# Optimization experiments

Hardware: AMD Instinct MI355X
Metric: run time of the kernel (lower is better)

The kernel has to match this reference:

```python
import jax, jax.numpy as jnp
import numpy as np
from jax.scipy.special import logsumexp

B, T, V, C, H, D, SPW, NC = 16, 256, 10000, 4096, 256, 256, 32, 128


def _res(x, w1, b1, w2, b2):
    # ResLayer: x + relu(lin2(relu(lin1(x))))
    return x + jax.nn.relu(jax.nn.relu(x @ w1 + b1) @ w2 + b2)


def _log_phi(x, proj):
    # Performer-style log random features for the softmax kernel (smp param.)
    return x @ proj - 0.5 * jnp.sum(x * x, -1, keepdims=True)


def _log_matmul_exp(a, b):
    # logits[i,j] = logsumexp_d(a[i,d] + b[j,d]), stable, via a single GEMM
    ma = jnp.max(a, -1, keepdims=True)
    mb = jnp.max(b, -1, keepdims=True)
    return jnp.log(jnp.exp(a - ma) @ jnp.exp(b - mb).T) + ma + mb.T


def setup_inputs() -> dict:
    key = jax.random.key(0)
    ks = jax.random.split(key, 12)
    s = 1.0 / np.sqrt(H)  # xavier-ish scale
    inp = {
        "text": jax.random.randint(ks[0], (B, T), 0, V),
        "start_emb": jax.random.normal(ks[1], (H,), jnp.float32) * s,
        "start_w": jax.random.normal(ks[2], (5, H, H), jnp.float32) * s,
        "start_b": jnp.zeros((5, H), jnp.float32),
        "state_emb": jax.random.normal(ks[3], (C, H), jnp.float32) * s,
        "next_state_emb": jax.random.normal(ks[4], (C, H), jnp.float32) * s,
        "preterminal_emb": jax.random.normal(ks[5], (C, H), jnp.float32) * s,
        "terminal_w": jax.random.normal(ks[6], (4, H, H), jnp.float32) * s,
        "terminal_b": jnp.zeros((4, H), jnp.float32),
        "terminal_emb": jax.random.normal(ks[7], (V, H), jnp.float32) * s,
        "projection": jax.random.normal(ks[8], (H, D), jnp.float32),
    }
    # brown-cluster style assignment: each cluster owns SPW disjoint states
    w2c = jax.random.randint(ks[9], (V,), 0, NC)
    c2s = jnp.arange(NC)[:, None] * SPW + jnp.arange(SPW)[None, :]
    inp["word2state"] = c2s[w2c]  # [V, SPW]
    return inp


def reference(text, word2state, start_emb, start_w, start_b, state_emb,
              next_state_emb, preterminal_emb, terminal_w, terminal_b,
              terminal_emb, projection):
    # --- start distribution (tie_start=True uses next_state_emb) ---
    fx = start_emb @ start_w[0] + start_b[0]
    fx = _res(fx, start_w[1], start_b[1], start_w[2], start_b[2])
    fx = _res(fx, start_w[3], start_b[3], start_w[4], start_b[4])
    lpy = _log_phi(next_state_emb, projection)                      # [C, D]
    start_lp = jax.nn.log_softmax(
        _log_matmul_exp(_log_phi(fx[None], projection), lpy)[0])    # [C]
    # --- transition: kernelized low-rank logits, row log-softmax ---
    trans_lp = jax.nn.log_softmax(
        _log_matmul_exp(_log_phi(state_emb, projection), lpy), -1)  # [C, C]
    # --- emission: terminal_mlp + sparse word2state mask ---
    fp = _res(preterminal_emb, terminal_w[0], terminal_b[0], terminal_w[1], terminal_b[1])
    fp = _res(fp, terminal_w[2], terminal_b[2], terminal_w[3], terminal_b[3])
    emit_logits = _log_matmul_exp(_log_phi(fp, projection),
                                  _log_phi(terminal_emb, projection))  # [C, V]
    rows = word2state.reshape(-1)
    cols = jnp.repeat(jnp.arange(V), SPW)
    mask = jnp.zeros((C, V), bool).at[rows, cols].set(True)
    emit_lp = jax.nn.log_softmax(jnp.where(mask, emit_logits, -1e30), -1)
    # --- log-space forward algorithm over clamped sparse states ---
    clamped = word2state[text]                          # [B, T, SPW]
    emit_bt = emit_lp[clamped, text[:, :, None]]        # [B, T, SPW]
    alpha0 = start_lp[clamped[:, 0]] + emit_bt[:, 0]    # [B, SPW]
    xs = (jnp.swapaxes(clamped[:, :-1], 0, 1),
          jnp.swapaxes(clamped[:, 1:], 0, 1),
          jnp.swapaxes(emit_bt[:, 1:], 0, 1))

    def step(alpha, x):
        cp, cc, em = x                                   # [B,SPW] each / em [B,SPW]
        tr = trans_lp[cp[:, :, None], cc[:, None, :]]    # [B, SPW, SPW]
        return logsumexp(alpha[:, :, None] + tr, axis=1) + em, None

    alpha, _ = jax.lax.scan(step, alpha0, xs)
    return logsumexp(alpha, -1)                          # [B] log evidence
```

## Files before the change

kernel.cpp:

```cpp
#include <hip/hip_runtime.h>

#define B_   16
#define T_   256
#define V_   10000
#define C_   4096
#define H_   256
#define NC_  128
#define CAP_ 224
#define MST  33
#define XST  257
#define HST  264

typedef __bf16 bf16x8 __attribute__((ext_vector_type(8)));
typedef unsigned short u16x8 __attribute__((ext_vector_type(8)));
typedef float  f32x4  __attribute__((ext_vector_type(4)));

__device__ inline unsigned short f2bf(float f){
  unsigned int u = __float_as_uint(f);
  u += 0x7FFFu + ((u >> 16) & 1u);
  return (unsigned short)(u >> 16);
}
__device__ inline float bf2f(unsigned short u){
  return __uint_as_float(((unsigned int)u) << 16);
}
__device__ inline f32x4 mfma16(bf16x8 a, bf16x8 b, f32x4 c){
  return __builtin_amdgcn_mfma_f32_16x16x32_bf16(a, b, c, 0, 0, 0);
}
__device__ inline bf16x8 load_cvt8(const float* p){
  u16x8 u;
  #pragma unroll
  for (int i = 0; i < 8; ++i) u[i] = f2bf(p[i]);
  return __builtin_bit_cast(bf16x8, u);
}
__device__ inline void zero_acc(f32x4 acc[2][4]){
  #pragma unroll
  for (int i = 0; i < 2; ++i)
    #pragma unroll
    for (int jx = 0; jx < 4; ++jx) acc[i][jx] = (f32x4){0.f,0.f,0.f,0.f};
}

__device__ inline void fx_accum(const float* __restrict__ W, const float* xh,
                                int j, float* __restrict__ Anext){
  int t = threadIdx.x;
  float p = 0.f;
  #pragma unroll
  for (int i = 0; i < 8; ++i)
    p = fmaf(xh[i], W[(size_t)(8*j + i)*256 + t], p);
  atomicAdd(&Anext[t], p);
}

__device__ inline void mm_A_gf32(const float* __restrict__ A, size_t lda_row0,
    const unsigned short* __restrict__ Bt, int w, int ln, f32x4 acc[2][4]){
  int m16 = ln & 15, q = ln >> 4, c0 = w*64;
  const float* a0 = A + lda_row0 + (size_t)m16*256 + q*8;
  const float* a1 = a0 + 16*256;
  const unsigned short* bp0 = Bt + (size_t)(c0 + m16)*256 + q*8;
  #pragma unroll
  for (int kt = 0; kt < 8; ++kt){
    bf16x8 af0 = load_cvt8(a0 + kt*32);
    bf16x8 af1 = load_cvt8(a1 + kt*32);
    #pragma unroll
    for (int cj = 0; cj < 4; ++cj){
      bf16x8 bfj = *(const bf16x8*)(bp0 + (size_t)cj*16*256 + kt*32);
      acc[0][cj] = mfma16(af0, bfj, acc[0][cj]);
// ... 201 lines not shown
  int tid = threadIdx.x;
  int w = tid >> 6, ln = tid & 63;
  int m16 = ln & 15, q = ln >> 4;
  int c0 = w*64;
  #pragma unroll
  for (int ri = 0; ri < 2; ++ri){
    #pragma unroll
    for (int r = 0; r < 4; ++r){
      int row = ri*16 + q*4 + r;
      float mv = -1e30f;
      #pragma unroll
      for (int cj = 0; cj < 4; ++cj){
        acc[ri][cj][r] -= lnrm[row];
        mv = fmaxf(mv, acc[ri][cj][r]);
      }
      #pragma unroll
      for (int d = 1; d < 16; d <<= 1) mv = fmaxf(mv, __shfl_xor(mv, d));
      if (m16 == 0) wrow[w][row] = mv;
    }
  }
  __syncthreads();
  #pragma unroll
  for (int ri = 0; ri < 2; ++ri){
    #pragma unroll
    for (int r = 0; r < 4; ++r){
      int row = ri*16 + q*4 + r;
      int grow = r0 + row;
      float m = fmaxf(fmaxf(wrow[0][row], wrow[1][row]), fmaxf(wrow[2][row], wrow[3][row]));
      if (grow < M){
        #pragma unroll
        for (int cj = 0; cj < 4; ++cj){
          int col = c0 + cj*16 + m16;
          E[(size_t)grow*256 + col] = f2bf(__expf(acc[ri][cj][r] - m));
        }
        if (w == 0 && m16 == 0) mr[grow] = m;
      }
    }
  }
}

__device__ inline void dev_phiE(const float* __restrict__ A,
    const unsigned short* __restrict__ projT, unsigned short* __restrict__ E,
    float* __restrict__ mr, int M, int r0, float* lnrm, float (*wrow)[32])
{
  int tid = threadIdx.x;
  int w = tid >> 6, ln = tid & 63;
  f32x4 acc[2][4];
  zero_acc(acc);
  phi_core(A, projT, r0, M, w, ln, acc, lnrm);
  __syncthreads();
  phiE_epilogue(acc, E, mr, M, r0, lnrm, wrow);
}

__global__ __launch_bounds__(256) void k_prep(
  const float* __restrict__ proj, const float* __restrict__ tw,
  unsigned short* __restrict__ projT, unsigned short* __restrict__ WT,
  const int* __restrict__ w2s, int* __restrict__ cnt, int* __restrict__ list,
  const float* __restrict__ se, const float* __restrict__ sw,
  float* __restrict__ Afx)
{
  int bx = blockIdx.x, tid = threadIdx.x;
  if (bx < 1280){
    int z = bx >> 8, dcol = bx & 255;
    const float* src = (z == 0) ? proj : (tw + (size_t)(z-1)*65536);
    unsigned short* dst = (z == 0) ? projT : (WT + (size_t)(z-1)*65536);
    dst[dcol*256 + tid] = f2bf(src[tid*256 + dcol]);
    return;
  }
  if (bx < 1320){
    int v = (bx - 1280)*256 + tid;
    if (v < V_){
      int k = w2s[v*32] >> 5;
      int pos = atomicAdd(&cnt[k], 1);
      if (pos < CAP_) list[k*CAP_ + pos] = v;
    }
    return;
  }
  int j = bx - 1320;
  float xh[8];
  #pragma unroll
  for (int i = 0; i < 8; ++i) xh[i] = se[8*j + i];
  fx_accum(sw, xh, j, Afx);
}

__global__ __launch_bounds__(256) void k_stageB(
  const float* __restrict__ pre_emb, const unsigned short* __restrict__ WT,
  const float* __restrict__ term_b,
  const unsigned short* __restrict__ projT,
  unsigned short* __restrict__ Epb, float* __restrict__ mpp,
  const float* __restrict__ next_emb, unsigned short* __restrict__ Ebp,
  float* __restrict__ S,
  const float* __restrict__ term_emb, unsigned short* __restrict__ Etb,
  float* __restrict__ mt,
  const float* __restrict__ sw, const float* __restrict__ sb,
  float* __restrict__ Afx)
{
  __shared__ __align__(16) float sX[32*XST];
  __shared__ __align__(16) unsigned short sHb[32*HST];
  __shared__ float lnrm[32];
  __shared__ float wrow[4][32];
  int bx = blockIdx.x, tid = threadIdx.x;
  int w = tid >> 6, ln = tid & 63;
  int m16 = ln & 15, q = ln >> 4;
  int c0 = w*64;
  if (bx < 128){
    int r0 = bx*32;
    f32x4 acc[2][4];
    zero_acc(acc);
    mm_A_gf32(pre_emb, (size_t)r0*256, WT, w, ln, acc);
    #pragma unroll
    for (int ri = 0; ri < 2; ++ri)
      #pragma unroll
      for (int cj = 0; cj < 4; ++cj)
        #pragma unroll
        for (int r = 0; r < 4; ++r){
          int row = ri*16 + q*4 + r, col = c0 + cj*16 + m16;
          sHb[row*HST + col] = f2bf(fmaxf(acc[ri][cj][r] + term_b[col], 0.f));
        }
    __syncthreads();
    zero_acc(acc);
    mm_A_ldsbf(sHb, WT + 65536, w, ln, acc);
    #pragma unroll
    for (int ri = 0; ri < 2; ++ri)
      #pragma unroll
      for (int cj = 0; cj < 4; ++cj)
        #pragma unroll
        for (int r = 0; r < 4; ++r){
          int row = ri*16 + q*4 + r, col = c0 + cj*16 + m16;
          float v = fmaxf(acc[ri][cj][r] + term_b[256 + col], 0.f);
          sX[row*XST + col] = v + pre_emb[(size_t)(r0 + row)*256 + col];
        }
    __syncthreads();
    zero_acc(acc);
    mm_A_ldsf32(sX, WT + 2*65536, w, ln, acc, nullptr);
    __syncthreads();
    #pragma unroll
    for (int ri = 0; ri < 2; ++ri)
      #pragma unroll
      for (int cj = 0; cj < 4; ++cj)
        #pragma unroll
        for (int r = 0; r < 4; ++r){
          int row = ri*16 + q*4 + r, col = c0 + cj*16 + m16;
          sHb[row*HST + col] = f2bf(fmaxf(acc[ri][cj][r] + term_b[512 + col], 0.f));
        }
    __syncthreads();
    zero_acc(acc);
    mm_A_ldsbf(sHb, WT + 3*65536, w, ln, acc);
    #pragma unroll
    for (int ri = 0; ri < 2; ++ri)
      #pragma unroll
      for (int cj = 0; cj < 4; ++cj)
        #pragma unroll
        for (int r = 0; r < 4; ++r){
          int row = ri*16 + q*4 + r, col = c0 + cj*16 + m16;
          sX[row*XST + col] += fmaxf(acc[ri][cj][r] + term_b[768 + col], 0.f);
        }
    __syncthreads();
    zero_acc(acc);
    mm_A_ldsf32(sX, projT, w, ln, acc, lnrm);
    __syncthreads();
    phiE_epilogue(acc, Epb, mpp, C_, r0, lnrm, wrow);
  } else if (bx < 256){
    dev_phiB(next_emb, projT, Ebp, S, (bx - 128)*32, lnrm);
  } else if (bx < 569){
    dev_phiE(term_emb, projT, Etb, mt, V_, (bx - 256)*32, lnrm, wrow);
  } else {
    int j = bx - 569;
    float xh[8];
    #pragma unroll
    for (int i = 0; i < 8; ++i){ int h = 8*j + i; xh[i] = Afx[h] + sb[h]; }
    fx_accum(sw + 65536, xh, j, Afx + 256);
  }
}

__global__ __launch_bounds__(256) void k_stageC(
  const float* __restrict__ state_emb, const unsigned short* __restrict__ projT,
  const float* __restrict__ S, unsigned short* __restrict__ Eap,
  const unsigned short* __restrict__ Epb, const float* __restrict__ mpp,
  const unsigned short* __restrict__ Etb, const float* __restrict__ mt,
  const int* __restrict__ cnt, const int* __restrict__ list,
  float* __restrict__ emit_col,
  const float* __restrict__ sw, const float* __restrict__ sb,
  float* __restrict__ Afx)
{
  __shared__ float lnrm[32];
  __shared__ float sS[256];
  __shared__ float wrow[4][32];
  __shared__ float wden[4][32];
  __shared__ float mtile[8][32];
  __shared__ float stile[8][32];
  __shared__ float mpl[32];
  __shared__ float denl[32];
  int bx = blockIdx.x, tid = threadIdx.x;
  if (bx < 128){
    dev_phiA(state_emb, projT, S, Eap, bx*32, lnrm, sS, wrow, wden);
    return;
  }
  if (bx >= 256){
    int j = bx - 256;
    float xh[8];
    #pragma unroll
    for (int i = 0; i < 8; ++i){ int h = 8*j + i; xh[i] = fmaxf(Afx[256 + h] + sb[256 + h], 0.f); }
    fx_accum(sw + 2*65536, xh, j, Afx + 512);
    return;
  }
  int k = bx - 128;
  int w = tid >> 6, ln = tid & 63;
  int m16 = ln & 15, q = ln >> 4;
  if (tid < 32) mpl[tid] = mpp[k*32 + tid];
  int n = cnt[k]; if (n > CAP_) n = CAP_;
  int nt = (n + 31) >> 5;
  const int* lp = list + k*CAP_;
  bf16x8 af0[8], af1[8];
  {
    const unsigned short* ap0 = Epb + (size_t)(k*32 + m16)*256 + q*8;
    const unsigned short* ap1 = ap0 + 16*256;
    #pragma unroll
    for (int kt = 0; kt < 8; ++kt){
      af0[kt] = *(const bf16x8*)(ap0 + kt*32);
      af1[kt] = *(const bf16x8*)(ap1 + kt*32);
    }
  }
  float lg[2][2][2][4];
  int   vj[2][2];
  #pragma unroll
  for (int u = 0; u < 2; ++u){
    int t = w + u*4;
    if (t >= nt) continue;
    int j0 = t*32 + m16, j1 = j0 + 16;
    int v0 = lp[(j0 < n) ? j0 : 0];
    int v1 = lp[(j1 < n) ? j1 : 0];
    vj[u][0] = v0; vj[u][1] = v1;
    float mt0 = (j0 < n) ? mt[v0] : 0.f;
    float mt1 = (j1 < n) ? mt[v1] : 0.f;
    const unsigned short* bp0 = Etb + (size_t)v0*256 + q*8;
    const unsigned short* bp1 = Etb + (size_t)v1*256 + q*8;
    f32x4 acc[2][2];
    #pragma unroll
    for (int mi = 0; mi < 2; ++mi)
      #pragma unroll
      for (int ni = 0; ni < 2; ++ni) acc[mi][ni] = (f32x4){0.f,0.f,0.f,0.f};
    #pragma unroll
    for (int kt = 0; kt < 8; ++kt){
      bf16x8 b0 = *(const bf16x8*)(bp0 + kt*32);
      bf16x8 b1 = *(const bf16x8*)(bp1 + kt*32);
      acc[0][0] = mfma16(af0[kt], b0, acc[0][0]);
      acc[0][1] = mfma16(af0[kt], b1, acc[0][1]);
      acc[1][0] = mfma16(af1[kt], b0, acc[1][0]);
      acc[1][1] = mfma16(af1[kt], b1, acc[1][1]);
    }
    #pragma unroll
    for (int mi = 0; mi < 2; ++mi){
      #pragma unroll
      for (int r = 0; r < 4; ++r){
        int row = mi*16 + q*4 + r;
        float l0 = (j0 < n) ? (__logf(acc[mi][0][r]) + mpl[row] + mt0) : -1e30f;
        float l1 = (j1 < n) ? (__logf(acc[mi][1][r]) + mpl[row] + mt1) : -1e30f;
        lg[u][mi][0][r] = l0;
        lg[u][mi][1][r] = l1;
        float mv = fmaxf(l0, l1);
        #pragma unroll
        for (int d = 1; d < 16; d <<= 1) mv = fmaxf(mv, __shfl_xor(mv, d));
        float se = __expf(l0 - mv) + __expf(l1 - mv);
        #pragma unroll
        for (int d = 1; d < 16; d <<= 1) se += __shfl_xor(se, d);
        if (m16 == 0){ mtile[t][row] = mv; stile[t][row] = se; }
      }
    }
  }
  __syncthreads();
  if (tid < 32){
    float gm = -1e30f;
    for (int t = 0; t < nt; ++t) gm = fmaxf(gm, mtile[t][tid]);
    float gs = 0.f;
    for (int t = 0; t < nt; ++t) gs += stile[t][tid]*__expf(mtile[t][tid] - gm);
// ... 56 lines not shown
    #pragma unroll
    for (int ni = 0; ni < 2; ++ni)
      #pragma unroll
      for (int r = 0; r < 4; ++r) mx = fmaxf(mx, acc[mi][ni][r]);
  #pragma unroll
  for (int d = 1; d < 64; d <<= 1) mx = fmaxf(mx, __shfl_xor(mx, d));
  float inv = 1.0f/mx;
  #pragma unroll
  for (int mi = 0; mi < 2; ++mi)
    #pragma unroll
    for (int ni = 0; ni < 2; ++ni)
      #pragma unroll
      for (int r = 0; r < 4; ++r)
        outp[(mi*16 + q*4 + r)*MST + ni*16 + m16] = acc[mi][ni][r]*inv;
  if (ln == 0) *sOut = sIn + __logf(mx);
}

__device__ inline void norm_store_g16(f32x4 acc[2][2], unsigned short* outp,
                                      float sIn, float* sOutG, int ln)
{
  int m16 = ln & 15, q = ln >> 4;
  float mx = 0.f;
  #pragma unroll
  for (int mi = 0; mi < 2; ++mi)
    #pragma unroll
    for (int ni = 0; ni < 2; ++ni)
      #pragma unroll
      for (int r = 0; r < 4; ++r) mx = fmaxf(mx, acc[mi][ni][r]);
  #pragma unroll
  for (int d = 1; d < 64; d <<= 1) mx = fmaxf(mx, __shfl_xor(mx, d));
  float inv = 1.0f/mx;
  #pragma unroll
  for (int mi = 0; mi < 2; ++mi)
    #pragma unroll
    for (int ni = 0; ni < 2; ++ni)
      #pragma unroll
      for (int r = 0; r < 4; ++r)
        outp[(mi*16 + q*4 + r)*32 + ni*16 + m16] = f2bf(acc[mi][ni][r]*inv);
  if (ln == 0) *sOutG = sIn + __logf(mx);
}

__device__ inline void prod32(const float* L0, const float* L1, float* outp,
                              float sIn, float* sOut, int ln)
{
  f32x4 acc[2][2];
  #pragma unroll
  for (int mi = 0; mi < 2; ++mi)
    #pragma unroll
    for (int ni = 0; ni < 2; ++ni) acc[mi][ni] = (f32x4){0.f,0.f,0.f,0.f};
  prod_acc(L0, L1, acc, ln);
  wave_norm_store(acc, outp, sIn, sOut, ln);
}

__global__ __launch_bounds__(512) void k_chunk(
  const unsigned short* __restrict__ Eap, const unsigned short* __restrict__ Ebp,
  const float* __restrict__ emit_col, const int* __restrict__ text,
  const int* __restrict__ w2s, unsigned short* __restrict__ Gm, float* __restrict__ Gs,
  const float* __restrict__ sw, const float* __restrict__ sb,
  float* __restrict__ Afx)
{
  __shared__ float bufL[8][32*MST];
  __shared__ float bufN[4][32*MST];
  __shared__ float sL[8], sN[4];
  int bx = blockIdx.x;
  int tid = threadIdx.x;
  if (bx >= 512){
    if (tid < 256){
      int j = bx - 512;
      float xh[8];
      #pragma unroll
      for (int i = 0; i < 8; ++i){
        int h = 8*j + i;
        float x0 = Afx[h] + sb[h];
        xh[i] = x0 + fmaxf(Afx[512 + h] + sb[512 + h], 0.f);
      }
      fx_accum(sw + 3*65536, xh, j, Afx + 768);
    }
    return;
  }
  int b = bx >> 5, ch = bx & 31;
  int w = tid >> 6, ln = tid & 63;
  int m16 = ln & 15, q = ln >> 4;
  {
    int s = ch*8 + w;
    float* outp = bufL[w];
    if (s >= 255){
      for (int i = ln; i < 32*32; i += 64){
        int r = i >> 5, c = i & 31;
        outp[r*MST + c] = (r == c) ? 1.f : 0.f;
      }
      if (ln == 0) sL[w] = 0.f;
    } else {
      int vp = text[b*256 + s], vc = text[b*256 + s + 1];
      int bp = w2s[vp*32], bq = w2s[vc*32];
      const unsigned short* a0 = Eap + (size_t)(bp + m16)*256 + q*8;
      const unsigned short* b0 = Ebp + (size_t)(bq + m16)*256 + q*8;
      f32x4 acc[2][2];
      #pragma unroll
      for (int mi = 0; mi < 2; ++mi)
        #pragma unroll
        for (int ni = 0; ni < 2; ++ni) acc[mi][ni] = (f32x4){0.f,0.f,0.f,0.f};
      #pragma unroll
      for (int kt = 0; kt < 8; ++kt){
        bf16x8 a_0 = *(const bf16x8*)(a0 + kt*32);
        bf16x8 a_1 = *(const bf16x8*)(a0 + 16*256 + kt*32);
        bf16x8 b_0 = *(const bf16x8*)(b0 + kt*32);
        bf16x8 b_1 = *(const bf16x8*)(b0 + 16*256 + kt*32);
        acc[0][0] = mfma16(a_0, b_0, acc[0][0]);
        acc[0][1] = mfma16(a_0, b_1, acc[0][1]);
        acc[1][0] = mfma16(a_1, b_0, acc[1][0]);
        acc[1][1] = mfma16(a_1, b_1, acc[1][1]);
      }
      float e0 = __expf(emit_col[(size_t)vc*32 + m16]);
      float e1 = __expf(emit_col[(size_t)vc*32 + 16 + m16]);
      #pragma unroll
      for (int mi = 0; mi < 2; ++mi)
        #pragma unroll
        for (int r = 0; r < 4; ++r){
          acc[mi][0][r] *= e0;
          acc[mi][1][r] *= e1;
        }
      wave_norm_store(acc, outp, 0.f, &sL[w], ln);
    }
  }
  __syncthreads();
  if (w < 4) prod32(bufL[2*w], bufL[2*w+1], bufN[w], sL[2*w] + sL[2*w+1], &sN[w], ln);
  __syncthreads();
  if (w < 2) prod32(bufN[2*w], bufN[2*w+1], bufL[w], sN[2*w] + sN[2*w+1], &sL[w], ln);
  __syncthreads();
  if (w == 0){
    f32x4 acc[2][2];
    #pragma unroll
    for (int mi = 0; mi < 2; ++mi)
      #pragma unroll
      for (int ni = 0; ni < 2; ++ni) acc[mi][ni] = (f32x4){0.f,0.f,0.f,0.f};
    prod_acc(bufL[0], bufL[1], acc, ln);
    norm_store_g16(acc, Gm + (size_t)bx*1024, sL[0] + sL[1], Gs + bx, ln);
  }
}

__device__ inline void load_mat16(const unsigned short* __restrict__ g,
                                  float* __restrict__ d, int ln){
  #pragma unroll
  for (int p = 0; p < 16; ++p){
    int idx = p*64 + ln;
    int r = idx >> 5, c = idx & 31;
    d[r*MST + c] = bf2f(g[idx]);
  }
}

__global__ __launch_bounds__(512) void k_root(
  const unsigned short* __restrict__ Gm, const float* __restrict__ Gs,
  const float* __restrict__ Afx, const float* __restrict__ sb,
  const float* __restrict__ sw, const float* __restrict__ proj,
  const float* __restrict__ S,
  const unsigned short* __restrict__ Ebp, const float* __restrict__ emit_col,
  const int* __restrict__ text, const int* __restrict__ w2s, float* __restrict__ out)
{
  __shared__ float W[8][3][32*MST];
  __shared__ float sW[8], sT[1];
  __shared__ float eafx[256], sX2[256], sH[256];
  __shared__ float gpart[2][256];
  __shared__ float red[4];
  int b = blockIdx.x;
  int tid = threadIdx.x;
  int w = tid >> 6, ln = tid & 63;
  int t = tid & 255, u = tid >> 8;
  if (tid < 256){
    float x0 = Afx[tid] + sb[tid];
    sX2[tid] = x0 + fmaxf(Afx[512 + tid] + sb[512 + tid], 0.f);
    sH[tid]  = fmaxf(Afx[768 + tid] + sb[768 + tid], 0.f);
  }
  __syncthreads();
  {
    float a = 0.f;
    const float* Wp = sw + 4*65536 + (size_t)(128*u)*256 + t;
    #pragma unroll 8
    for (int h = 0; h < 128; ++h) a = fmaf(sH[128*u + h], Wp[(size_t)h*256], a);
    gpart[u][t] = a;
  }
  __syncthreads();
  if (tid < 256){
    float A4 = gpart[0][t] + gpart[1][t];
    float x4 = sX2[t] + fmaxf(A4 + sb[1024 + t], 0.f);
    sX2[t] = x4;
    float v2 = x4*x4;
    #pragma unroll
    for (int d = 1; d < 64; d <<= 1) v2 += __shfl_xor(v2, d);
    if ((t & 63) == 0) red[t >> 6] = v2;
  }
  __syncthreads();
  float nx = red[0] + red[1] + red[2] + red[3];
  {
    float a = 0.f;
    const float* Pp = proj + (size_t)(128*u)*256 + t;
    #pragma unroll 8
    for (int h = 0; h < 128; ++h) a = fmaf(sX2[128*u + h], Pp[(size_t)h*256], a);
    gpart[u][t] = a;
  }
  __syncthreads();
  float pxv = 0.f;
  if (tid < 256){
    pxv = gpart[0][t] + gpart[1][t] - 0.5f*nx;
    float m2 = pxv;
    #pragma unroll
    for (int d = 1; d < 64; d <<= 1) m2 = fmaxf(m2, __shfl_xor(m2, d));
    if ((t & 63) == 0) red[t >> 6] = m2;
  }
  __syncthreads();
  float m2g = fmaxf(fmaxf(red[0], red[1]), fmaxf(red[2], red[3]));
  if (tid < 256) eafx[t] = __expf(pxv - m2g);
  __syncthreads();
  const unsigned short* G = Gm + ((size_t)(b*32 + w*4))*1024;
  const float* gs = Gs + b*32 + w*4;
  load_mat16(G,        W[w][0], ln);
  load_mat16(G + 1024, W[w][1], ln);
  prod32(W[w][0], W[w][1], W[w][2], gs[0] + gs[1], &sW[w], ln);
  load_mat16(G + 2048, W[w][0], ln);
  prod32(W[w][2], W[w][0], W[w][1], sW[w] + gs[2], &sW[w], ln);
  load_mat16(G + 3072, W[w][0], ln);
  prod32(W[w][1], W[w][0], W[w][2], sW[w] + gs[3], &sW[w], ln);
  __syncthreads();
  if (w == 0){
    float sAcc = sW[0];
    const float* cur = W[0][2];
    int dsel = 0;
    for (int j = 1; j < 8; ++j){
      float* dst = dsel ? W[0][1] : W[0][0];
      prod32(cur, W[j][2], dst, sAcc + sW[j], &sT[0], ln);
      sAcc = sT[0];
      cur = dst;
      dsel ^= 1;
    }
    float part = 0.f;
    for (int d = ln; d < 256; d += 64) part = fmaf(eafx[d], S[d], part);
    #pragma unroll
    for (int d2 = 1; d2 < 64; d2 <<= 1) part += __shfl_xor(part, d2);
    float dfx = part;
    int v0 = text[b*256];
    int k0 = w2s[v0*32];
    int j = ln & 31, h = ln >> 5;
    const unsigned short* er = Ebp + (size_t)(k0 + j)*256;
    float dot = 0.f;
    for (int d = h*128; d < h*128 + 128; ++d)
      dot = fmaf(eafx[d], bf2f(er[d]), dot);
    dot += __shfl_xor(dot, 32);
    float z0 = __logf(dot) + emit_col[(size_t)v0*32 + j];
    float mz = z0;
    #pragma unroll
    for (int d2 = 1; d2 < 32; d2 <<= 1) mz = fmaxf(mz, __shfl_xor(mz, d2));
    float an = __expf(z0 - mz);
    float cs = 0.f;
    for (int i = h*16; i < h*16 + 16; ++i)
      cs = fmaf(__shfl(an, i), cur[i*MST + j], cs);
    cs += __shfl_xor(cs, 32);
    float tot = cs;
    #pragma unroll
    for (int d2 = 1; d2 < 32; d2 <<= 1) tot += __shfl_xor(tot, d2);
    if (ln == 0) out[b] = __logf(tot) + mz + sAcc - __logf(dfx);
  }
}

extern "C" void kernel_launch(void* const* d_in, const int* in_sizes, int n_in,
                              void* d_out, int out_size, void* d_ws, size_t ws_size,
                              hipStream_t stream)
{
  (void)in_sizes; (void)n_in; (void)out_size; (void)ws_size;
  const int*   text      = (const int*)  d_in[0];
  const float* start_emb = (const float*)d_in[1];
  const float* start_w   = (const float*)d_in[2];
  const float* start_b   = (const float*)d_in[3];
  const float* state_emb = (const float*)d_in[4];
  const float* next_emb  = (const float*)d_in[5];
  const float* pre_emb   = (const float*)d_in[6];
  const float* term_w    = (const float*)d_in[7];
  const float* term_b    = (const float*)d_in[8];
  const float* term_emb  = (const float*)d_in[9];
  const float* proj      = (const float*)d_in[10];
  const int*   w2s       = (const int*)  d_in[11];
  float* out = (float*)d_out;

  char* base = (char*)d_ws;
  size_t off = 0;
  auto alloc = [&](size_t bytes)->char*{
    char* p = base + off;
    off += (bytes + 255) & ~(size_t)255;
    return p;
  };
  int*   cnt = (int*)  alloc(128*4);
  float* Afx = (float*)alloc(4*256*4);
  float* S   = (float*)alloc(256*4);
  unsigned short* projT = (unsigned short*)alloc((size_t)65536*2);
  unsigned short* WT    = (unsigned short*)alloc((size_t)4*65536*2);
  unsigned short* Epb = (unsigned short*)alloc((size_t)C_*256*2);
  float* mpp  = (float*)alloc((size_t)C_*4);
  unsigned short* Etb = (unsigned short*)alloc((size_t)V_*256*2);
  float* mt   = (float*)alloc((size_t)V_*4);
  unsigned short* Eap = (unsigned short*)alloc((size_t)C_*256*2);
  unsigned short* Ebp = (unsigned short*)alloc((size_t)C_*256*2);
  int* list = (int*)alloc((size_t)128*CAP_*4);
  float* emit_col = (float*)alloc((size_t)V_*32*4);
  unsigned short* Gm = (unsigned short*)alloc((size_t)512*1024*2);
  float* Gs = (float*)alloc((size_t)512*4);

  (void)hipMemsetAsync(cnt, 0, 512 + 4096 + 1024, stream);

  k_prep<<<1352, 256, 0, stream>>>(proj, term_w, projT, WT, w2s, cnt, list,
                                   start_emb, start_w, Afx);
  k_stageB<<<601, 256, 0, stream>>>(pre_emb, WT, term_b, projT, Epb, mpp,
                                    next_emb, Ebp, S, term_emb, Etb, mt,
                                    start_w, start_b, Afx);
  k_stageC<<<288, 256, 0, stream>>>(state_emb, projT, S, Eap,
                                    Epb, mpp, Etb, mt, cnt, list, emit_col,
                                    start_w, start_b, Afx);
  k_chunk<<<544, 512, 0, stream>>>(Eap, Ebp, emit_col, text, w2s, Gm, Gs,
                                   start_w, start_b, Afx);
  k_root<<<16, 512, 0, stream>>>(Gm, Gs, Afx, start_b, start_w, proj, S,
                                 Ebp, emit_col, text, w2s, out);
}
```

Baseline: 202.8 us.

## Fuse five stage kernels into one cooperative persistent kernel with grid syncs

Replaces the five separate launches (prep, stageB, stageC, chunk, root) with a single cooperative kernel of 256 blocks. Each block loops over the work items of every phase, and grid.sync separates the phases, so launch gaps and inter-kernel drain are removed. The chunk and root stages are reworked from 512 to 256 threads, so each wave now builds two transition matrices and the product tree is reorganised. The risks are lower parallelism per phase, since 256 blocks stride over up to 1352 items, and the cost of the grid barriers. A fallback path keeps separate launches if the cooperative launch fails.

```diff
diff --git a/kernel.cpp b/kernel.cpp
--- a/kernel.cpp
+++ b/kernel.cpp
@@ -1,15 +1,17 @@
 #include <hip/hip_runtime.h>
+#include <hip/hip_cooperative_groups.h>
+namespace cg = cooperative_groups;
 
 #define B_   16
 #define T_   256
 #define V_   10000
 #define C_   4096
-#define H_   256
 #define NC_  128
 #define CAP_ 224
 #define MST  33
 #define XST  257
 #define HST  264
+#define SMEM_BYTES 51840
 
 typedef __bf16 bf16x8 __attribute__((ext_vector_type(8)));
 typedef unsigned short u16x8 __attribute__((ext_vector_type(8)));
@@ -317,159 +319,87 @@
   phiE_epilogue(acc, E, mr, M, r0, lnrm, wrow);
 }
 
-__global__ __launch_bounds__(256) void k_prep(
-  const float* __restrict__ proj, const float* __restrict__ tw,
-  unsigned short* __restrict__ projT, unsigned short* __restrict__ WT,
-  const int* __restrict__ w2s, int* __restrict__ cnt, int* __restrict__ list,
-  const float* __restrict__ se, const float* __restrict__ sw,
-  float* __restrict__ Afx)
-{
-  int bx = blockIdx.x, tid = threadIdx.x;
-  if (bx < 1280){
-    int z = bx >> 8, dcol = bx & 255;
-    const float* src = (z == 0) ? proj : (tw + (size_t)(z-1)*65536);
-    unsigned short* dst = (z == 0) ? projT : (WT + (size_t)(z-1)*65536);
-    dst[dcol*256 + tid] = f2bf(src[tid*256 + dcol]);
-    return;
-  }
-  if (bx < 1320){
-    int v = (bx - 1280)*256 + tid;
-    if (v < V_){
-      int k = w2s[v*32] >> 5;
-      int pos = atomicAdd(&cnt[k], 1);
-      if (pos < CAP_) list[k*CAP_ + pos] = v;
-    }
-    return;
-  }
-  int j = bx - 1320;
-  float xh[8];
-  #pragma unroll
-  for (int i = 0; i < 8; ++i) xh[i] = se[8*j + i];
-  fx_accum(sw, xh, j, Afx);
-}
-
-__global__ __launch_bounds__(256) void k_stageB(
-  const float* __restrict__ pre_emb, const unsigned short* __restrict__ WT,
-  const float* __restrict__ term_b,
-  const unsigned short* __restrict__ projT,
-  unsigned short* __restrict__ Epb, float* __restrict__ mpp,
-  const float* __restrict__ next_emb, unsigned short* __restrict__ Ebp,
-  float* __restrict__ S,
-  const float* __restrict__ term_emb, unsigned short* __restrict__ Etb,
-  float* __restrict__ mt,
-  const float* __restrict__ sw, const float* __restrict__ sb,
-  float* __restrict__ Afx)
-{
-  __shared__ __align__(16) float sX[32*XST];
-  __shared__ __align__(16) unsigned short sHb[32*HST];
-  __shared__ float lnrm[32];
-  __shared__ float wrow[4][32];
-  int bx = blockIdx.x, tid = threadIdx.x;
+__device__ inline void dev_mlpAll(const float* __restrict__ pre_emb,
+    const unsigned short* __restrict__ WT, const float* __restrict__ term_b,
+    const unsigned short* __restrict__ projT,
+    unsigned short* __restrict__ Epb, float* __restrict__ mpp, int r0, char* smem)
+{
+  float* sX = (float*)smem;
+  unsigned short* sHb = (unsigned short*)(smem + 32896);
+  float* lnrm = (float*)(smem + 49792);
+  float (*wrow)[32] = (float(*)[32])(smem + 49920);
+  int tid = threadIdx.x;
   int w = tid >> 6, ln = tid & 63;
   int m16 = ln & 15, q = ln >> 4;
   int c0 = w*64;
-  if (bx < 128){
-    int r0 = bx*32;
-    f32x4 acc[2][4];
-    zero_acc(acc);
-    mm_A_gf32(pre_emb, (size_t)r0*256, WT, w, ln, acc);
-    #pragma unroll
-    for (int ri = 0; ri < 2; ++ri)
-      #pragma unroll
-      for (int cj = 0; cj < 4; ++cj)
-        #pragma unroll
-        for (int r = 0; r < 4; ++r){
-          int row = ri*16 + q*4 + r, col = c0 + cj*16 + m16;
-          sHb[row*HST + col] = f2bf(fmaxf(acc[ri][cj][r] + term_b[col], 0.f));
-        }
-    __syncthreads();
-    zero_acc(acc);
-    mm_A_ldsbf(sHb, WT + 65536, w, ln, acc);
-    #pragma unroll
-    for (int ri = 0; ri < 2; ++ri)
-      #pragma unroll
-      for (int cj = 0; cj < 4; ++cj)
-        #pragma unroll
-        for (int r = 0; r < 4; ++r){
-          int row = ri*16 + q*4 + r, col = c0 + cj*16 + m16;
-          float v = fmaxf(acc[ri][cj][r] + term_b[256 + col], 0.f);
-          sX[row*XST + col] = v + pre_emb[(size_t)(r0 + row)*256 + col];
-        }
-    __syncthreads();
-    zero_acc(acc);
-    mm_A_ldsf32(sX, WT + 2*65536, w, ln, acc, nullptr);
-    __syncthreads();
-    #pragma unroll
-    for (int ri = 0; ri < 2; ++ri)
-      #pragma unroll
-      for (int cj = 0; cj < 4; ++cj)
-        #pragma unroll
-        for (int r = 0; r < 4; ++r){
-          int row = ri*16 + q*4 + r, col = c0 + cj*16 + m16;
-          sHb[row*HST + col] = f2bf(fmaxf(acc[ri][cj][r] + term_b[512 + col], 0.f));
-        }
-    __syncthreads();
-    zero_acc(acc);
-    mm_A_ldsbf(sHb, WT + 3*65536, w, ln, acc);
-    #pragma unroll
-    for (int ri = 0; ri < 2; ++ri)
-      #pragma unroll
-      for (int cj = 0; cj < 4; ++cj)
-        #pragma unroll
-        for (int r = 0; r < 4; ++r){
-          int row = ri*16 + q*4 + r, col = c0 + cj*16 + m16;
-          sX[row*XST + col] += fmaxf(acc[ri][cj][r] + term_b[768 + col], 0.f);
-        }
-    __syncthreads();
-    zero_acc(acc);
-    mm_A_ldsf32(sX, projT, w, ln, acc, lnrm);
-    __syncthreads();
-    phiE_epilogue(acc, Epb, mpp, C_, r0, lnrm, wrow);
-  } else if (bx < 256){
-    dev_phiB(next_emb, projT, Ebp, S, (bx - 128)*32, lnrm);
-  } else if (bx < 569){
-    dev_phiE(term_emb, projT, Etb, mt, V_, (bx - 256)*32, lnrm, wrow);
-  } else {
-    int j = bx - 569;
-    float xh[8];
-    #pragma unroll
-    for (int i = 0; i < 8; ++i){ int h = 8*j + i; xh[i] = Afx[h] + sb[h]; }
-    fx_accum(sw + 65536, xh, j, Afx + 256);
-  }
-}
-
-__global__ __launch_bounds__(256) void k_stageC(
-  const float* __restrict__ state_emb, const unsigned short* __restrict__ projT,
-  const float* __restrict__ S, unsigned short* __restrict__ Eap,
-  const unsigned short* __restrict__ Epb, const float* __restrict__ mpp,
-  const unsigned short* __restrict__ Etb, const float* __restrict__ mt,
-  const int* __restrict__ cnt, const int* __restrict__ list,
-  float* __restrict__ emit_col,
-  const float* __restrict__ sw, const float* __restrict__ sb,
-  float* __restrict__ Afx)
-{
-  __shared__ float lnrm[32];
-  __shared__ float sS[256];
-  __shared__ float wrow[4][32];
-  __shared__ float wden[4][32];
-  __shared__ float mtile[8][32];
-  __shared__ float stile[8][32];
-  __shared__ float mpl[32];
-  __shared__ float denl[32];
-  int bx = blockIdx.x, tid = threadIdx.x;
-  if (bx < 128){
-    dev_phiA(state_emb, projT, S, Eap, bx*32, lnrm, sS, wrow, wden);
-    return;
-  }
-  if (bx >= 256){
-    int j = bx - 256;
-    float xh[8];
-    #pragma unroll
-    for (int i = 0; i < 8; ++i){ int h = 8*j + i; xh[i] = fmaxf(Afx[256 + h] + sb[256 + h], 0.f); }
-    fx_accum(sw + 2*65536, xh, j, Afx + 512);
-    return;
-  }
-  int k = bx - 128;
+  f32x4 acc[2][4];
+  zero_acc(acc);
+  mm_A_gf32(pre_emb, (size_t)r0*256, WT, w, ln, acc);
+  #pragma unroll
+  for (int ri = 0; ri < 2; ++ri)
+    #pragma unroll
+    for (int cj = 0; cj < 4; ++cj)
+      #pragma unroll
+      for (int r = 0; r < 4; ++r){
+        int row = ri*16 + q*4 + r, col = c0 + cj*16 + m16;
+        sHb[row*HST + col] = f2bf(fmaxf(acc[ri][cj][r] + term_b[col], 0.f));
+      }
+  __syncthreads();
+  zero_acc(acc);
+  mm_A_ldsbf(sHb, WT + 65536, w, ln, acc);
+  #pragma unroll
+  for (int ri = 0; ri < 2; ++ri)
+    #pragma unroll
+    for (int cj = 0; cj < 4; ++cj)
+      #pragma unroll
+      for (int r = 0; r < 4; ++r){
+        int row = ri*16 + q*4 + r, col = c0 + cj*16 + m16;
+        float v = fmaxf(acc[ri][cj][r] + term_b[256 + col], 0.f);
+        sX[row*XST + col] = v + pre_emb[(size_t)(r0 + row)*256 + col];
+      }
+  __syncthreads();
+  zero_acc(acc);
+  mm_A_ldsf32(sX, WT + 2*65536, w, ln, acc, nullptr);
+  __syncthreads();
+  #pragma unroll
+  for (int ri = 0; ri < 2; ++ri)
+    #pragma unroll
+    for (int cj = 0; cj < 4; ++cj)
+      #pragma unroll
+      for (int r = 0; r < 4; ++r){
+        int row = ri*16 + q*4 + r, col = c0 + cj*16 + m16;
+        sHb[row*HST + col] = f2bf(fmaxf(acc[ri][cj][r] + term_b[512 + col], 0.f));
+      }
+  __syncthreads();
+  zero_acc(acc);
+  mm_A_ldsbf(sHb, WT + 3*65536, w, ln, acc);
+  #pragma unroll
+  for (int ri = 0; ri < 2; ++ri)
+    #pragma unroll
+    for (int cj = 0; cj < 4; ++cj)
+      #pragma unroll
+      for (int r = 0; r < 4; ++r){
+        int row = ri*16 + q*4 + r, col = c0 + cj*16 + m16;
+        sX[row*XST + col] += fmaxf(acc[ri][cj][r] + term_b[768 + col], 0.f);
+      }
+  __syncthreads();
+  zero_acc(acc);
+  mm_A_ldsf32(sX, projT, w, ln, acc, lnrm);
+  __syncthreads();
+  phiE_epilogue(acc, Epb, mpp, C_, r0, lnrm, wrow);
+}
+
+__device__ inline void dev_emit(int k,
+    const unsigned short* __restrict__ Epb, const float* __restrict__ mpp,
+    const unsigned short* __restrict__ Etb, const float* __restrict__ mt,
+    const int* __restrict__ cnt, const int* __restrict__ list,
+    float* __restrict__ emit_col, char* smem)
+{
+  float (*mtile)[32] = (float(*)[32])smem;
+  float (*stile)[32] = (float(*)[32])(smem + 1024);
+  float* mpl  = (float*)(smem + 2048);
+  float* denl = (float*)(smem + 2176);
+  int tid = threadIdx.x;
   int w = tid >> 6, ln = tid & 63;
   int m16 = ln & 15, q = ln >> 4;
   if (tid < 32) mpl[tid] = mpp[k*32 + tid];
@@ -486,6 +416,7 @@
       af1[kt] = *(const bf16x8*)(ap1 + kt*32);
     }
   }
+  __syncthreads();
   float lg[2][2][2][4];
   int   vj[2][2];
   #pragma unroll
@@ -648,44 +579,127 @@
   wave_norm_store(acc, outp, sIn, sOut, ln);
 }
 
-__global__ __launch_bounds__(512) void k_chunk(
-  const unsigned short* __restrict__ Eap, const unsigned short* __restrict__ Ebp,
-  const float* __restrict__ emit_col, const int* __restrict__ text,
-  const int* __restrict__ w2s, unsigned short* __restrict__ Gm, float* __restrict__ Gs,
-  const float* __restrict__ sw, const float* __restrict__ sb,
-  float* __restrict__ Afx)
-{
-  __shared__ float bufL[8][32*MST];
-  __shared__ float bufN[4][32*MST];
-  __shared__ float sL[8], sN[4];
-  int bx = blockIdx.x;
+__device__ inline void load_mat16(const unsigned short* __restrict__ g,
+                                  float* __restrict__ d, int ln){
+  #pragma unroll
+  for (int p = 0; p < 16; ++p){
+    int idx = p*64 + ln;
+    int r = idx >> 5, c = idx & 31;
+    d[r*MST + c] = bf2f(g[idx]);
+  }
+}
+
+__device__ inline void phase0_item(int it,
+  const float* proj, const float* tw, unsigned short* projT, unsigned short* WT,
+  const int* w2s, int* cnt, int* list, const float* se, const float* sw, float* Afx)
+{
   int tid = threadIdx.x;
-  if (bx >= 512){
-    if (tid < 256){
-      int j = bx - 512;
-      float xh[8];
-      #pragma unroll
-      for (int i = 0; i < 8; ++i){
-        int h = 8*j + i;
-        float x0 = Afx[h] + sb[h];
-        xh[i] = x0 + fmaxf(Afx[512 + h] + sb[512 + h], 0.f);
-      }
-      fx_accum(sw + 3*65536, xh, j, Afx + 768);
-    }
+  if (it < 1280){
+    int z = it >> 8, dcol = it & 255;
+    const float* src = (z == 0) ? proj : (tw + (size_t)(z-1)*65536);
+    unsigned short* dst = (z == 0) ? projT : (WT + (size_t)(z-1)*65536);
+    dst[dcol*256 + tid] = f2bf(src[tid*256 + dcol]);
+  } else if (it < 1320){
+    int v = (it - 1280)*256 + tid;
+    if (v < V_){
+      int k = w2s[v*32] >> 5;
+      int pos = atomicAdd(&cnt[k], 1);
+      if (pos < CAP_) list[k*CAP_ + pos] = v;
+    }
+  } else {
+    int j = it - 1320;
+    float xh[8];
+    #pragma unroll
+    for (int i = 0; i < 8; ++i) xh[i] = se[8*j + i];
+    fx_accum(sw, xh, j, Afx);
+  }
+}
+
+__device__ inline void phase1_item(int it,
+  const float* pre_emb, const unsigned short* WT, const float* term_b,
+  const unsigned short* projT, unsigned short* Epb, float* mpp,
+  const float* next_emb, unsigned short* Ebp, float* S,
+  const float* term_emb, unsigned short* Etb, float* mt,
+  const float* sw, const float* sb, float* Afx, char* smem)
+{
+  if (it < 128){
+    dev_mlpAll(pre_emb, WT, term_b, projT, Epb, mpp, it*32, smem);
+  } else if (it < 256){
+    float* lnrm = (float*)smem;
+    dev_phiB(next_emb, projT, Ebp, S, (it - 128)*32, lnrm);
+  } else if (it < 569){
+    float* lnrm = (float*)smem;
+    float (*wrow)[32] = (float(*)[32])(smem + 128);
+    dev_phiE(term_emb, projT, Etb, mt, V_, (it - 256)*32, lnrm, wrow);
+  } else {
+    int j = it - 569;
+    float xh[8];
+    #pragma unroll
+    for (int i = 0; i < 8; ++i){ int h = 8*j + i; xh[i] = Afx[h] + sb[h]; }
+    fx_accum(sw + 65536, xh, j, Afx + 256);
+  }
+}
+
+__device__ inline void phase2_item(int it,
+  const float* state_emb, const unsigned short* projT, const float* S,
+  unsigned short* Eap, const unsigned short* Epb, const float* mpp,
+  const unsigned short* Etb, const float* mt, const int* cnt, const int* list,
+  float* emit_col, const float* sw, const float* sb, float* Afx, char* smem)
+{
+  if (it < 128){
+    float* lnrm = (float*)smem;
+    float* sS = (float*)(smem + 128);
+    float (*wrowA)[32] = (float(*)[32])(smem + 1152);
+    float (*wden)[32]  = (float(*)[32])(smem + 1664);
+    dev_phiA(state_emb, projT, S, Eap, it*32, lnrm, sS, wrowA, wden);
+  } else if (it < 256){
+    dev_emit(it - 128, Epb, mpp, Etb, mt, cnt, list, emit_col, smem);
+  } else {
+    int j = it - 256;
+    float xh[8];
+    #pragma unroll
+    for (int i = 0; i < 8; ++i){ int h = 8*j + i; xh[i] = fmaxf(Afx[256 + h] + sb[256 + h], 0.f); }
+    fx_accum(sw + 2*65536, xh, j, Afx + 512);
+  }
+}
+
+__device__ inline void phase3_item(int it,
+  const unsigned short* Eap, const unsigned short* Ebp, const float* emit_col,
+  const int* text, const int* w2s, unsigned short* Gm, float* Gs,
+  const float* sw, const float* sb, float* Afx, char* smem)
+{
+  int tid = threadIdx.x;
+  if (it >= 512){
+    int j = it - 512;
+    float xh[8];
+    #pragma unroll
+    for (int i = 0; i < 8; ++i){
+      int h = 8*j + i;
+      float x0 = Afx[h] + sb[h];
+      xh[i] = x0 + fmaxf(Afx[512 + h] + sb[512 + h], 0.f);
+    }
+    fx_accum(sw + 3*65536, xh, j, Afx + 768);
     return;
   }
-  int b = bx >> 5, ch = bx & 31;
+  float* bufL = (float*)smem;
+  float* bufN = (float*)(smem + 33792);
+  float* sL = (float*)(smem + 50688);
+  float* sN = sL + 8;
+  float* sT = sN + 4;
+  int b = it >> 5, ch = it & 31;
   int w = tid >> 6, ln = tid & 63;
   int m16 = ln & 15, q = ln >> 4;
-  {
-    int s = ch*8 + w;
-    float* outp = bufL[w];
+  #pragma unroll
+  for (int u = 0; u < 2; ++u){
+    int l = 2*w + u;
+    int s = ch*8 + l;
+    float* outp = bufL + l*1056;
     if (s >= 255){
       for (int i = ln; i < 32*32; i += 64){
         int r = i >> 5, c = i & 31;
         outp[r*MST + c] = (r == c) ? 1.f : 0.f;
       }
-      if (ln == 0) sL[w] = 0.f;
+      if (ln == 0) sL[l] = 0.f;
     } else {
       int vp = text[b*256 + s], vc = text[b*256 + s + 1];
       int bp = w2s[vp*32], bq = w2s[vc*32];
@@ -716,118 +730,115 @@
           acc[mi][0][r] *= e0;
           acc[mi][1][r] *= e1;
         }
-      wave_norm_store(acc, outp, 0.f, &sL[w], ln);
-    }
-  }
-  __syncthreads();
-  if (w < 4) prod32(bufL[2*w], bufL[2*w+1], bufN[w], sL[2*w] + sL[2*w+1], &sN[w], ln);
-  __syncthreads();
-  if (w < 2) prod32(bufN[2*w], bufN[2*w+1], bufL[w], sN[2*w] + sN[2*w+1], &sL[w], ln);
+      wave_norm_store(acc, outp, 0.f, &sL[l], ln);
+    }
+  }
+  prod32(bufL + 2*w*1056, bufL + (2*w+1)*1056, bufN + w*1056,
+         sL[2*w] + sL[2*w+1], &sN[w], ln);
   __syncthreads();
   if (w == 0){
+    prod32(bufN, bufN + 1056, bufL, sN[0] + sN[1], &sT[0], ln);
+    prod32(bufL, bufN + 2*1056, bufL + 1056, sT[0] + sN[2], &sT[1], ln);
     f32x4 acc[2][2];
     #pragma unroll
     for (int mi = 0; mi < 2; ++mi)
       #pragma unroll
       for (int ni = 0; ni < 2; ++ni) acc[mi][ni] = (f32x4){0.f,0.f,0.f,0.f};
-    prod_acc(bufL[0], bufL[1], acc, ln);
-    norm_store_g16(acc, Gm + (size_t)bx*1024, sL[0] + sL[1], Gs + bx, ln);
-  }
-}
-
-__device__ inline void load_mat16(const unsigned short* __restrict__ g,
-                                  float* __restrict__ d, int ln){
-  #pragma unroll
-  for (int p = 0; p < 16; ++p){
-    int idx = p*64 + ln;
-    int r = idx >> 5, c = idx & 31;
-    d[r*MST + c] = bf2f(g[idx]);
-  }
-}
-
-__global__ __launch_bounds__(512) void k_root(
-  const unsigned short* __restrict__ Gm, const float* __restrict__ Gs,
-  const float* __restrict__ Afx, const float* __restrict__ sb,
-  const float* __restrict__ sw, const float* __restrict__ proj,
-  const float* __restrict__ S,
-  const unsigned short* __restrict__ Ebp, const float* __restrict__ emit_col,
-  const int* __restrict__ text, const int* __restrict__ w2s, float* __restrict__ out)
-{
-  __shared__ float W[8][3][32*MST];
-  __shared__ float sW[8], sT[1];
-  __shared__ float eafx[256], sX2[256], sH[256];
-  __shared__ float gpart[2][256];
-  __shared__ float red[4];
-  int b = blockIdx.x;
+    prod_acc(bufL + 1056, bufN + 3*1056, acc, ln);
+    norm_store_g16(acc, Gm + (size_t)it*1024, sT[1] + sN[3], Gs + it, ln);
+  }
+}
+
+__device__ inline void phase4_block(int b,
+  const unsigned short* Gm, const float* Gs, const float* Afx, const float* sb,
+  const float* sw, const float* proj, const float* S,
+  const unsigned short* Ebp, const float* emit_col, const int* text,
+  const int* w2s, float* out, char* smem)
+{
+  float* Wb   = (float*)smem;
+  float* sW   = (float*)(smem + 50688);
+  float* sTr  = sW + 4;
+  float* eafx = (float*)(smem + 50720);
+  float* red  = (float*)(smem + 51744);
   int tid = threadIdx.x;
   int w = tid >> 6, ln = tid & 63;
-  int t = tid & 255, u = tid >> 8;
-  if (tid < 256){
+  {
+    float* scr = (float*)smem;
+    float* sX2 = scr; float* sH = scr + 256; float* sX4 = scr + 512;
     float x0 = Afx[tid] + sb[tid];
     sX2[tid] = x0 + fmaxf(Afx[512 + tid] + sb[512 + tid], 0.f);
     sH[tid]  = fmaxf(Afx[768 + tid] + sb[768 + tid], 0.f);
-  }
-  __syncthreads();
+    __syncthreads();
+    float a0=0.f,a1=0.f,a2=0.f,a3=0.f;
+    const float* Wp = sw + 4*65536 + tid;
+    #pragma unroll 4
+    for (int h = 0; h < 256; h += 4){
+      a0 = fmaf(sH[h+0], Wp[(size_t)(h+0)*256], a0);
+      a1 = fmaf(sH[h+1], Wp[(size_t)(h+1)*256], a1);
+      a2 = fmaf(sH[h+2], Wp[(size_t)(h+2)*256], a2);
+      a3 = fmaf(sH[h+3], Wp[(size_t)(h+3)*256], a3);
+    }
+    float A4 = (a0+a1)+(a2+a3);
+    float x4 = sX2[tid] + fmaxf(A4 + sb[1024 + tid], 0.f);
+    sX4[tid] = x4;
+    float v2 = x4*x4;
+    #pragma unroll
+    for (int d = 1; d < 64; d <<= 1) v2 += __shfl_xor(v2, d);
+    if ((tid & 63) == 0) red[tid >> 6] = v2;
+    __syncthreads();
+    float nx = red[0]+red[1]+red[2]+red[3];
+    a0=a1=a2=a3=0.f;
+    const float* Pp = proj + tid;
+    #pragma unroll 4
+    for (int h = 0; h < 256; h += 4){
+      a0 = fmaf(sX4[h+0], Pp[(size_t)(h+0)*256], a0);
+      a1 = fmaf(sX4[h+1], Pp[(size_t)(h+1)*256], a1);
+      a2 = fmaf(sX4[h+2], Pp[(size_t)(h+2)*256], a2);
+      a3 = fmaf(sX4[h+3], Pp[(size_t)(h+3)*256], a3);
+    }
+    float pxv = (a0+a1)+(a2+a3) - 0.5f*nx;
+    __syncthreads();
+    float m2 = pxv;
+    #pragma unroll
+    for (int d = 1; d < 64; d <<= 1) m2 = fmaxf(m2, __shfl_xor(m2, d));
+    if ((tid & 63) == 0) red[tid >> 6] = m2;
+    __syncthreads();
+    float m2g = fmaxf(fmaxf(red[0], red[1]), fmaxf(red[2], red[3]));
+    eafx[tid] = __expf(pxv - m2g);
+    __syncthreads();
+  }
   {
-    float a = 0.f;
-    const float* Wp = sw + 4*65536 + (size_t)(128*u)*256 + t;
-    #pragma unroll 8
-    for (int h = 0; h < 128; ++h) a = fmaf(sH[128*u + h], Wp[(size_t)h*256], a);
-    gpart[u][t] = a;
-  }
-  __syncthreads();
-  if (tid < 256){
-    float A4 = gpart[0][t] + gpart[1][t];
-    float x4 = sX2[t] + fmaxf(A4 + sb[1024 + t], 0.f);
-    sX2[t] = x4;
-    float v2 = x4*x4;
-    #pragma unroll
-    for (int d = 1; d < 64; d <<= 1) v2 += __shfl_xor(v2, d);
-    if ((t & 63) == 0) red[t >> 6] = v2;
-  }
-  __syncthreads();
-  float nx = red[0] + red[1] + red[2] + red[3];
-  {
-    float a = 0.f;
-    const float* Pp = proj + (size_t)(128*u)*256 + t;
-    #pragma unroll 8
-    for (int h = 0; h < 128; ++h) a = fmaf(sX2[128*u + h], Pp[(size_t)h*256], a);
-    gpart[u][t] = a;
-  }
-  __syncthreads();
-  float pxv = 0.f;
-  if (tid < 256){
-    pxv = gpart[0][t] + gpart[1][t] - 0.5f*nx;
-    float m2 = pxv;
-    #pragma unroll
-    for (int d = 1; d < 64; d <<= 1) m2 = fmaxf(m2, __shfl_xor(m2, d));
-    if ((t & 63) == 0) red[t >> 6] = m2;
-  }
-  __syncthreads();
-  float m2g = fmaxf(fmaxf(red[0], red[1]), fmaxf(red[2], red[3]));
-  if (tid < 256) eafx[t] = __expf(pxv - m2g);
-  __syncthreads();
-  const unsigned short* G = Gm + ((size_t)(b*32 + w*4))*1024;
-  const float* gs = Gs + b*32 + w*4;
-  load_mat16(G,        W[w][0], ln);
-  load_mat16(G + 1024, W[w][1], ln);
-  prod32(W[w][0], W[w][1], W[w][2], gs[0] + gs[1], &sW[w], ln);
-  load_mat16(G + 2048, W[w][0], ln);
-  prod32(W[w][2], W[w][0], W[w][1], sW[w] + gs[2], &sW[w], ln);
-  load_mat16(G + 3072, W[w][0], ln);
-  prod32(W[w][1], W[w][0], W[w][2], sW[w] + gs[3], &sW[w], ln);
+    const unsigned short* G = Gm + ((size_t)(b*32 + w*8))*1024;
+    const float* gs = Gs + b*32 + w*8;
+    float* W0 = Wb + (w*3 + 0)*1056;
+    float* W1 = Wb + (w*3 + 1)*1056;
+    float* W2 = Wb + (w*3 + 2)*1056;
+    load_mat16(G,        W0, ln);
+    load_mat16(G + 1024, W1, ln);
+    prod32(W0, W1, W2, gs[0] + gs[1], &sW[w], ln);
+    int cur = 2;
+    for (int j = 2; j < 8; ++j){
+      load_mat16(G + (size_t)j*1024, W0, ln);
+      int dst = (cur == 2) ? 1 : 2;
+      float* curp = (cur == 2) ? W2 : W1;
+      float* dstp = (dst == 2) ? W2 : W1;
+      prod32(curp, W0, dstp, sW[w] + gs[j], &sW[w], ln);
+      cur = dst;
+    }
+  }
   __syncthreads();
   if (w == 0){
-    float sAcc = sW[0];
-    const float* cur = W[0][2];
-    int dsel = 0;
-    for (int j = 1; j < 8; ++j){
-      float* dst = dsel ? W[0][1] : W[0][0];
-      prod32(cur, W[j][2], dst, sAcc + sW[j], &sT[0], ln);
-      sAcc = sT[0];
-      cur = dst;
-      dsel ^= 1;
-    }
+    float* N0 = Wb + 2*1056;
+    float* N1 = Wb + (1*3 + 2)*1056;
+    float* N2 = Wb + (2*3 + 2)*1056;
+    float* N3 = Wb + (3*3 + 2)*1056;
+    float* T0 = Wb;
+    float* T1 = Wb + 1056;
+    prod32(N0, N1, T0, sW[0] + sW[1], &sTr[0], ln);
+    prod32(T0, N2, T1, sTr[0] + sW[2], &sTr[0], ln);
+    prod32(T1, N3, T0, sTr[0] + sW[3], &sTr[0], ln);
+    float sAcc = sTr[0];
+    const float* cur = T0;
     float part = 0.f;
     for (int d = ln; d < 256; d += 64) part = fmaf(eafx[d], S[d], part);
     #pragma unroll
@@ -855,6 +866,93 @@
     for (int d2 = 1; d2 < 32; d2 <<= 1) tot += __shfl_xor(tot, d2);
     if (ln == 0) out[b] = __logf(tot) + mz + sAcc - __logf(dfx);
   }
+}
+
+__global__ __launch_bounds__(256) void k_mega(
+  const float* proj, const float* tw, unsigned short* projT, unsigned short* WT,
+  const int* w2s, int* cnt, int* list, const float* se, const float* sw,
+  const float* sb, float* Afx, const float* pre_emb, const float* term_b,
+  unsigned short* Epb, float* mpp, const float* next_emb, unsigned short* Ebp,
+  float* S, const float* term_emb, unsigned short* Etb, float* mt,
+  const float* state_emb, unsigned short* Eap, float* emit_col,
+  const int* text, unsigned short* Gm, float* Gs, float* out)
+{
+  __shared__ __align__(16) char smem[SMEM_BYTES];
+  cg::grid_group grid = cg::this_grid();
+  int nb = gridDim.x;
+  for (int it = blockIdx.x; it < 1352; it += nb)
+    phase0_item(it, proj, tw, projT, WT, w2s, cnt, list, se, sw, Afx);
+  grid.sync();
+  for (int it = blockIdx.x; it < 601; it += nb){
+    __syncthreads();
+    phase1_item(it, pre_emb, WT, term_b, projT, Epb, mpp, next_emb, Ebp, S,
+                term_emb, Etb, mt, sw, sb, Afx, smem);
+  }
+  grid.sync();
+  for (int it = blockIdx.x; it < 288; it += nb){
+    __syncthreads();
+    phase2_item(it, state_emb, projT, S, Eap, Epb, mpp, Etb, mt, cnt, list,
+                emit_col, sw, sb, Afx, smem);
+  }
+  grid.sync();
+  for (int it = blockIdx.x; it < 544; it += nb){
+    __syncthreads();
+    phase3_item(it, Eap, Ebp, emit_col, text, w2s, Gm, Gs, sw, sb, Afx, smem);
+  }
+  grid.sync();
+  if (blockIdx.x < B_)
+    phase4_block(blockIdx.x, Gm, Gs, Afx, sb, sw, proj, S, Ebp, emit_col,
+                 text, w2s, out, smem);
+}
+
+__global__ __launch_bounds__(256) void k_p0(
+  const float* proj, const float* tw, unsigned short* projT, unsigned short* WT,
+  const int* w2s, int* cnt, int* list, const float* se, const float* sw, float* Afx)
+{
+  phase0_item(blockIdx.x, proj, tw, projT, WT, w2s, cnt, list, se, sw, Afx);
+}
+
+__global__ __launch_bounds__(256) void k_p1(
+  const float* pre_emb, const unsigned short* WT, const float* term_b,
+  const unsigned short* projT, unsigned short* Epb, float* mpp,
+  const float* next_emb, unsigned short* Ebp, float* S,
+  const float* term_emb, unsigned short* Etb, float* mt,
+  const float* sw, const float* sb, float* Afx)
+{
+  __shared__ __align__(16) char smem[SMEM_BYTES];
+  phase1_item(blockIdx.x, pre_emb, WT, term_b, projT, Epb, mpp, next_emb, Ebp,
+              S, term_emb, Etb, mt, sw, sb, Afx, smem);
+}
+
+__global__ __launch_bounds__(256) void k_p2(
+  const float* state_emb, const unsigned short* projT, const float* S,
+  unsigned short* Eap, const unsigned short* Epb, const float* mpp,
+  const unsigned short* Etb, const float* mt, const int* cnt, const int* list,
+  float* emit_col, const float* sw, const float* sb, float* Afx)
+{
+  __shared__ __align__(16) char smem[4096];
+  phase2_item(blockIdx.x, state_emb, projT, S, Eap, Epb, mpp, Etb, mt, cnt,
+              list, emit_col, sw, sb, Afx, smem);
+}
+
+__global__ __launch_bounds__(256) void k_p3(
+  const unsigned short* Eap, const unsigned short* Ebp, const float* emit_col,
+  const int* text, const int* w2s, unsigned short* Gm, float* Gs,
+  const float* sw, const float* sb, float* Afx)
+{
+  __shared__ __align__(16) char smem[SMEM_BYTES];
+  phase3_item(blockIdx.x, Eap, Ebp, emit_col, text, w2s, Gm, Gs, sw, sb, Afx, smem);
+}
+
+__global__ __launch_bounds__(256) void k_p4(
+  const unsigned short* Gm, const float* Gs, const float* Afx, const float* sb,
+  const float* sw, const float* proj, const float* S,
+  const unsigned short* Ebp, const float* emit_col, const int* text,
+  const int* w2s, float* out)
+{
+  __shared__ __align__(16) char smem[SMEM_BYTES];
+  phase4_block(blockIdx.x, Gm, Gs, Afx, sb, sw, proj, S, Ebp, emit_col,
+               text, w2s, out, smem);
 }
 
 extern "C" void kernel_launch(void* const* d_in, const int* in_sizes, int n_in,
@@ -901,16 +999,29 @@
 
   (void)hipMemsetAsync(cnt, 0, 512 + 4096 + 1024, stream);
 
-  k_prep<<<1352, 256, 0, stream>>>(proj, term_w, projT, WT, w2s, cnt, list,
+  void* kargs[] = {
+    (void*)&proj, (void*)&term_w, (void*)&projT, (void*)&WT, (void*)&w2s,
+    (void*)&cnt, (void*)&list, (void*)&start_emb, (void*)&start_w,
+    (void*)&start_b, (void*)&Afx, (void*)&pre_emb, (void*)&term_b,
+    (void*)&Epb, (void*)&mpp, (void*)&next_emb, (void*)&Ebp, (void*)&S,
+    (void*)&term_emb, (void*)&Etb, (void*)&mt, (void*)&state_emb,
+    (void*)&Eap, (void*)&emit_col, (void*)&text, (void*)&Gm, (void*)&Gs,
+    (void*)&out
+  };
+  hipError_t err = hipLaunchCooperativeKernel((void*)k_mega, dim3(256),
+                                              dim3(256), kargs, 0, stream);
+  if (err != hipSuccess){
+    (void)hipGetLastError();
+    k_p0<<<1352, 256, 0, stream>>>(proj, term_w, projT, WT, w2s, cnt, list,
                                    start_emb, start_w, Afx);
-  k_stageB<<<601, 256, 0, stream>>>(pre_emb, WT, term_b, projT, Epb, mpp,
-                                    next_emb, Ebp, S, term_emb, Etb, mt,
-                                    start_w, start_b, Afx);
-  k_stageC<<<288, 256, 0, stream>>>(state_emb, projT, S, Eap,
-                                    Epb, mpp, Etb, mt, cnt, list, emit_col,
-                                    start_w, start_b, Afx);
-  k_chunk<<<544, 512, 0, stream>>>(Eap, Ebp, emit_col, text, w2s, Gm, Gs,
-                                   start_w, start_b, Afx);
-  k_root<<<16, 512, 0, stream>>>(Gm, Gs, Afx, start_b, start_w, proj, S,
+    k_p1<<<601, 256, 0, stream>>>(pre_emb, WT, term_b, projT, Epb, mpp,
+                                  next_emb, Ebp, S, term_emb, Etb, mt,
+                                  start_w, start_b, Afx);
+    k_p2<<<288, 256, 0, stream>>>(state_emb, projT, S, Eap, Epb, mpp, Etb, mt,
+                                  cnt, list, emit_col, start_w, start_b, Afx);
+    k_p3<<<544, 256, 0, stream>>>(Eap, Ebp, emit_col, text, w2s, Gm, Gs,
+                                  start_w, start_b, Afx);
+    k_p4<<<16, 256, 0, stream>>>(Gm, Gs, Afx, start_b, start_w, proj, S,
                                  Ebp, emit_col, text, w2s, out);
-}
+  }
+}
```

New measurement: 438.2 us. 116% more time.
